# Performance work log

Hardware: AMD Instinct MI355X
Metric: run time of the kernel (lower is better)

The kernel has to match this reference:

```python
import math
import jax, jax.numpy as jnp
import numpy as np

D_MODEL = 512
N_HEADS = 8
NUM_PHASES = 3
LN_EPS = 1e-5


def setup_inputs() -> dict:
    key = jax.random.key(0)
    ks = jax.random.split(key, 8)
    B, T, C = 4, 2048, D_MODEL
    s = 1.0 / math.sqrt(C)  # keep activations sane
    return {
        "x": jax.random.normal(ks[0], (B, T, C), dtype=jnp.float32),
        "Wq_w": jax.random.normal(ks[1], (C, C), dtype=jnp.float32) * s,
        "Wq_b": jnp.zeros((C,), dtype=jnp.float32),
        "Wk_w": jax.random.normal(ks[2], (C, C), dtype=jnp.float32) * s,
        "Wk_b": jnp.zeros((C,), dtype=jnp.float32),
        "Wv_w": jax.random.normal(ks[3], (C, C), dtype=jnp.float32) * s,
        "Wv_b": jnp.zeros((C,), dtype=jnp.float32),
        "Wo_w": jax.random.normal(ks[4], (C, C), dtype=jnp.float32) * s,
        "Wo_b": jnp.zeros((C,), dtype=jnp.float32),
        "phase_bias": jax.random.normal(ks[5], (NUM_PHASES, NUM_PHASES), dtype=jnp.float32),
        "ln_g": jnp.ones((C,), dtype=jnp.float32),
        "ln_b": jnp.zeros((C,), dtype=jnp.float32),
    }


def reference(x, Wq_w, Wq_b, Wk_w, Wk_b, Wv_w, Wv_b, Wo_w, Wo_b, phase_bias, ln_g, ln_b):
    B, T, C = x.shape
    H, dk = N_HEADS, C // N_HEADS
    # torch Linear: y = x @ W.T + b
    Q = (x @ Wq_w.T + Wq_b).reshape(B, T, H, dk).transpose(0, 2, 1, 3)
    K = (x @ Wk_w.T + Wk_b).reshape(B, T, H, dk).transpose(0, 2, 1, 3)
    V = (x @ Wv_w.T + Wv_b).reshape(B, T, H, dk).transpose(0, 2, 1, 3)
    scores = jnp.einsum('bhqd,bhkd->bhqk', Q, K) / math.sqrt(dk)  # [B,H,T,T]
    # tiled additive phase bias (num_phases <= T)
    n_tiles = (T + NUM_PHASES - 1) // NUM_PHASES
    bias = jnp.tile(phase_bias, (n_tiles, n_tiles))[:T, :T]  # [T,T]
    scores = scores + bias  # broadcast over B,H
    attn = jax.nn.softmax(scores, axis=-1)  # dropout is identity in eval
    ctx = jnp.einsum('bhqk,bhkd->bhqd', attn, V)
    ctx = ctx.transpose(0, 2, 1, 3).reshape(B, T, C)
    out = ctx @ Wo_w.T + Wo_b
    y = out + x
    mu = jnp.mean(y, axis=-1, keepdims=True)
    var = jnp.mean(jnp.square(y - mu), axis=-1, keepdims=True)
    return (y - mu) / jnp.sqrt(var + LN_EPS) * ln_g + ln_b
```

## Files before the change

### kernel.cpp

```cpp
#include <hip/hip_runtime.h>

typedef __attribute__((ext_vector_type(8))) short s16x8;
typedef __attribute__((ext_vector_type(8))) unsigned short u16x8;
typedef __attribute__((ext_vector_type(4))) float f32x4;
typedef unsigned short u16;
typedef unsigned int u32;

#define T_ 2048
#define C_ 512
#define H_ 8
#define DKP 96
#define LOG2E 1.44269504088896340736f
#define QSCALE 0.18033688011112042f

__device__ __forceinline__ u16 f2b(float f) {
  u32 u = __float_as_uint(f);
  return (u16)((u + 0x7FFFu + ((u >> 16) & 1u)) >> 16);
}

__device__ __forceinline__ float b2f(u16 b) {
  return __uint_as_float(((u32)b) << 16);
}

__device__ __forceinline__ u16x8 cvt8(float4 a, float4 b) {
  u16x8 o;
  o[0] = f2b(a.x); o[1] = f2b(a.y); o[2] = f2b(a.z); o[3] = f2b(a.w);
  o[4] = f2b(b.x); o[5] = f2b(b.y); o[6] = f2b(b.z); o[7] = f2b(b.w);
  return o;
}

__device__ __forceinline__ f32x4 mfma16(s16x8 a, s16x8 b, f32x4 c) {
  return __builtin_amdgcn_mfma_f32_16x16x32_bf16(a, b, c, 0, 0, 0);
}

__global__ __launch_bounds__(256) void k_convert(
    const float* __restrict__ x,
    const float* __restrict__ wq, const float* __restrict__ wk,
    const float* __restrict__ wv, const float* __restrict__ wo,
    const float* __restrict__ bq, const float* __restrict__ bk,
    const float* __restrict__ bv, const float* __restrict__ pb,
    u16* __restrict__ xb, u16* __restrict__ wcat, u16* __restrict__ wo16,
    float* __restrict__ bcat, u16* __restrict__ qp, u16* __restrict__ kp)
{
  const int blk = blockIdx.x, tid = threadIdx.x;
  if (blk < 2048) {
    int i = blk * 2048 + tid * 8;
    float4 a = *(const float4*)(x + i);
    float4 b = *(const float4*)(x + i + 4);
    *(u16x8*)(xb + i) = cvt8(a, b);
  } else if (blk < 2432) {
    int bi = blk - 2048;
    const float* src; int off;
    if (bi < 128)      { src = wq; off = bi * 2048; }
    else if (bi < 256) { src = wk; off = (bi - 128) * 2048; }
    else               { src = wv; off = (bi - 256) * 2048; }
    int i = off + tid * 8;
    float4 a = *(const float4*)(src + i);
    float4 b = *(const float4*)(src + i + 4);
    *(u16x8*)(wcat + bi * 2048 + tid * 8) = cvt8(a, b);
  } else if (blk < 2560) {
    int i = (blk - 2432) * 2048 + tid * 8;
    float4 a = *(const float4*)(wo + i);
    float4 b = *(const float4*)(wo + i + 4);
    *(u16x8*)(wo16 + i) = cvt8(a, b);
  } else if (blk == 2560) {
    if (tid < 192) {
      int i = tid * 8;
      const float* src; int off;
      if (i < 512)       { src = bq; off = i; }
      else if (i < 1024) { src = bk; off = i - 512; }
      else               { src = bv; off = i - 1024; }
      *(float4*)(bcat + i)     = *(const float4*)(src + off);
      *(float4*)(bcat + i + 4) = *(const float4*)(src + off + 4);
    }
  } else if (blk < 3585) {
    int e = (blk - 2561) * 2048 + tid * 8;
    int row = e >> 5, cc = e & 31;
    int tp = (row & 2047) % 3;
    u16x8 o;
    #pragma unroll
    for (int j = 0; j < 8; ++j) {
      int cidx = cc + j;
      o[j] = (cidx < 3) ? ((tp == cidx) ? (u16)0x3F80 : (u16)0) : (u16)0;
    }
    *(u16x8*)(qp + row * DKP + 64 + cc) = o;
  } else {
    int e = (blk - 3585) * 2048 + tid * 8;
    int row = e >> 5, cc = e & 31;
    int tp = (row & 2047) % 3;
    u16x8 o;
    #pragma unroll
    for (int j = 0; j < 8; ++j) {
      int cidx = cc + j;
      o[j] = (cidx < 3) ? f2b(pb[cidx * 3 + tp] * LOG2E) : (u16)0;
    }
    *(u16x8*)(kp + row * DKP + 64 + cc) = o;
  }
}

template<int MODE>
__global__ __launch_bounds__(256) void k_gemm(
    const u16* __restrict__ A, const u16* __restrict__ Bw,
    const float* __restrict__ bias,
    u16* __restrict__ qp, u16* __restrict__ kp, u16* __restrict__ vtmp,
    float* __restrict__ yout)
{
  const int n0 = blockIdx.x * 128;
  const int m0 = blockIdx.y * 128;
  const int tid = threadIdx.x;
  const int lane = tid & 63, wid = tid >> 6;
  const int g = lane >> 4, c = lane & 15;
  const int wm = wid >> 1, wn = wid & 1;

  __shared__ alignas(16) u16 As[128 * 40];
  __shared__ alignas(16) u16 Bs[128 * 40];

  f32x4 acc[4][4];
  #pragma unroll
  for (int i = 0; i < 4; ++i)
    #pragma unroll
    for (int j = 0; j < 4; ++j) acc[i][j] = f32x4{0.f, 0.f, 0.f, 0.f};

  const int srow = tid >> 1;
  const int sj = (tid & 1) * 16;
  const u16* Ag = A + (m0 + srow) * C_ + sj;
  const u16* Bg = Bw + (n0 + srow) * C_ + sj;
  u16* Al = As + srow * 40 + sj;
  u16* Bl = Bs + srow * 40 + sj;

  s16x8 a0 = *(const s16x8*)(Ag);
  s16x8 a1 = *(const s16x8*)(Ag + 8);
  s16x8 b0 = *(const s16x8*)(Bg);
  s16x8 b1 = *(const s16x8*)(Bg + 8);

  const int KT = C_ / 32;
  for (int kt = 0; kt < KT; ++kt) {
    __syncthreads();
    *(s16x8*)(Al) = a0; *(s16x8*)(Al + 8) = a1;
    *(s16x8*)(Bl) = b0; *(s16x8*)(Bl + 8) = b1;
    __syncthreads();
    if (kt + 1 < KT) {
      a0 = *(const s16x8*)(Ag + (kt + 1) * 32);
      a1 = *(const s16x8*)(Ag + (kt + 1) * 32 + 8);
      b0 = *(const s16x8*)(Bg + (kt + 1) * 32);
      b1 = *(const s16x8*)(Bg + (kt + 1) * 32 + 8);
    }
    s16x8 af[4], bf[4];
    #pragma unroll
    for (int mf = 0; mf < 4; ++mf)
      af[mf] = *(const s16x8*)(As + (wm * 64 + mf * 16 + c) * 40 + g * 8);
    #pragma unroll
    for (int nf = 0; nf < 4; ++nf)
      bf[nf] = *(const s16x8*)(Bs + (wn * 64 + nf * 16 + c) * 40 + g * 8);
    #pragma unroll
    for (int mf = 0; mf < 4; ++mf)
      #pragma unroll
      for (int nf = 0; nf < 4; ++nf)
        acc[mf][nf] = mfma16(af[mf], bf[nf], acc[mf][nf]);
  }

  float bv4[4];
  #pragma unroll
  for (int nf = 0; nf < 4; ++nf) bv4[nf] = bias[n0 + wn * 64 + nf * 16 + c];

  #pragma unroll
  for (int mf = 0; mf < 4; ++mf) {
    const int btb = m0 + wm * 64 + mf * 16 + g * 4;
    #pragma unroll
    for (int nf = 0; nf < 4; ++nf) {
      const int n = n0 + wn * 64 + nf * 16 + c;
      #pragma unroll
      for (int r = 0; r < 4; ++r) {
        float v = acc[mf][nf][r] + bv4[nf];
        const int row = btb + r;
        if (MODE == 1) {
          yout[row * C_ + n] = v;
        } else {
          if (n < 512) {
            const int hh = n >> 6, d = n & 63;
            const int bb = row >> 11, t = row & 2047;
            qp[((bb * H_ + hh) * T_ + t) * DKP + d] = f2b(v * QSCALE);
          } else if (n < 1024) {
            const int nn = n - 512;
            const int hh = nn >> 6, d = nn & 63;
            const int bb = row >> 11, t = row & 2047;
            kp[((bb * H_ + hh) * T_ + t) * DKP + d] = f2b(v);
          } else {
            vtmp[row * C_ + (n - 1024)] = f2b(v);
          }
        }
      }
    }
  }
}

__global__ __launch_bounds__(256) void k_vtrans(const u16* __restrict__ vtmp,
                                                u16* __restrict__ vt)
{
  const int t0 = blockIdx.x * 64;
  const int bh = blockIdx.y;
  const int b = bh >> 3, h = bh & 7;
  const int tid = threadIdx.x;
  __shared__ alignas(16) u16 tile[64 * 72];
  #pragma unroll
  for (int it = 0; it < 2; ++it) {
    int task = tid + it * 256;
    int r = task >> 3, cj = task & 7;
    int pr = (r & 32) | (((r & 15) << 1) | ((r >> 4) & 1));
    u16x8 v = *(const u16x8*)(vtmp + (b * T_ + t0 + r) * C_ + h * 64 + cj * 8);
    #pragma unroll
    for (int j = 0; j < 8; ++j) tile[(cj * 8 + j) * 72 + pr] = v[j];
  }
  __syncthreads();
  #pragma unroll
  for (int it = 0; it < 2; ++it) {
    int task = tid + it * 256;
    int d = task >> 3, cj = task & 7;
    u16x8 o = *(const u16x8*)(tile + d * 72 + cj * 8);
    *(u16x8*)(vt + (bh * 80 + d) * T_ + t0 + cj * 8) = o;
  }
  if (tid < 128) {
    int d = 64 + (tid >> 3), cj = tid & 7;
    u16 val = (d == 64) ? (u16)0x3F80 : (u16)0;
    u16x8 o;
    #pragma unroll
    for (int j = 0; j < 8; ++j) o[j] = val;
    *(u16x8*)(vt + (bh * 80 + d) * T_ + t0 + cj * 8) = o;
  }
}

__global__ __launch_bounds__(256) void k_attn(
    const u16* __restrict__ qp, const u16* __restrict__ kp,
    const u16* __restrict__ vt, u16* __restrict__ pc0, u16* __restrict__ pc1,
    float* __restrict__ pl)
{
  const int lid = blockIdx.x;
  const int xcd = lid & 7, j = lid >> 3;
  const int gsel = j >> 4, qblk = j & 15;
  const int bhz = xcd * 8 + gsel;
  const int bh = bhz >> 1, z = bhz & 1;

  const int tid = threadIdx.x, wid = tid >> 6, lane = tid & 63;
  const int g = lane >> 4, c = lane & 15;

  __shared__ alignas(16) u16 Ks[32 * 104];
  __shared__ alignas(16) u16 Vs[80 * 40];
  __shared__ alignas(16) u16 Ps[4][32 * 40];

  const int q0 = qblk * 128 + wid * 32;
  const u16* qpb = qp + (bh * T_ + q0) * DKP;
  s16x8 qfr[2][3];
  #pragma unroll
  for (int a = 0; a < 2; ++a)
    #pragma unroll
    for (int ks = 0; ks < 3; ++ks)
      qfr[a][ks] = *(const s16x8*)(qpb + (a * 16 + c) * DKP + ks * 32 + g * 8);

  f32x4 acc[2][5];
  #pragma unroll
  for (int a = 0; a < 2; ++a)
    #pragma unroll
    for (int df = 0; df < 5; ++df) acc[a][df] = f32x4{0.f, 0.f, 0.f, 0.f};

  const int r_k0 = tid / 12, j_k0 = tid % 12;
  const int r_k1 = (256 + tid) / 12, j_k1 = (256 + tid) % 12;
  const bool k2 = tid < 128;
  const u16* kpb = kp + (bh * T_ + z * 1024) * DKP;
  u16* kl0 = Ks + r_k0 * 104 + j_k0 * 8;
  u16* kl1 = Ks + r_k1 * 104 + j_k1 * 8;
  const int ko0 = r_k0 * DKP + j_k0 * 8;
  const int ko1 = r_k1 * DKP + j_k1 * 8;

  const int r_v0 = tid >> 2, j_v0 = tid & 3;
  const bool v2 = tid < 64;
  const int r_v1 = 64 + (tid >> 2), j_v1 = tid & 3;
  const u16* vtb = vt + bh * 80 * T_ + z * 1024;
  u16* vl0 = Vs + r_v0 * 40 + j_v0 * 8;
  u16* vl1 = Vs + r_v1 * 40 + j_v1 * 8;
  const int vo0 = r_v0 * T_ + j_v0 * 8;
  const int vo1 = r_v1 * T_ + j_v1 * 8;

  s16x8 kc0 = *(const s16x8*)(kpb + ko0);
  s16x8 kc1 = {}; if (k2) kc1 = *(const s16x8*)(kpb + ko1);
  s16x8 vc0 = *(const s16x8*)(vtb + vo0);
  s16x8 vc1 = {}; if (v2) vc1 = *(const s16x8*)(vtb + vo1);

  for (int kt = 0; kt < 32; ++kt) {
    __syncthreads();
    *(s16x8*)kl0 = kc0;
    if (k2) *(s16x8*)kl1 = kc1;
    *(s16x8*)vl0 = vc0;
    if (v2) *(s16x8*)vl1 = vc1;
    __syncthreads();
    if (kt < 31) {
      const int off = (kt + 1) * 32;
      kc0 = *(const s16x8*)(kpb + off * DKP + ko0);
      if (k2) kc1 = *(const s16x8*)(kpb + off * DKP + ko1);
      vc0 = *(const s16x8*)(vtb + off + vo0);
      if (v2) vc1 = *(const s16x8*)(vtb + off + vo1);
    }

    f32x4 s2[2][2];
    #pragma unroll
    for (int a = 0; a < 2; ++a)
      #pragma unroll
      for (int kf = 0; kf < 2; ++kf) s2[a][kf] = f32x4{0.f, 0.f, 0.f, 0.f};
    #pragma unroll
    for (int kf = 0; kf < 2; ++kf)
      #pragma unroll
      for (int ks = 0; ks < 3; ++ks) {
        s16x8 kfrag = *(const s16x8*)(Ks + (kf * 16 + c) * 104 + (ks * 4 + g) * 8);
        s2[0][kf] = mfma16(qfr[0][ks], kfrag, s2[0][kf]);
        s2[1][kf] = mfma16(qfr[1][ks], kfrag, s2[1][kf]);
      }

    #pragma unroll
    for (int a = 0; a < 2; ++a) {
      u32* pw = (u32*)(Ps[wid] + (a * 16 + g * 4) * 40) + c;
      #pragma unroll
      for (int r = 0; r < 4; ++r) {
        u32 b0 = __float_as_uint(exp2f(s2[a][0][r]));
        u32 b1 = __float_as_uint(exp2f(s2[a][1][r]));
        pw[r * 20] = ((b0 + 0x8000u) >> 16) | (((b1 + 0x8000u) >> 16) << 16);
      }
    }

    s16x8 pf0 = *(const s16x8*)(Ps[wid] + c * 40 + g * 8);
    s16x8 pf1 = *(const s16x8*)(Ps[wid] + (16 + c) * 40 + g * 8);
    #pragma unroll
    for (int df = 0; df < 5; ++df) {
      s16x8 vfrag = *(const s16x8*)(Vs + (df * 16 + c) * 40 + g * 8);
      acc[0][df] = mfma16(pf0, vfrag, acc[0][df]);
      acc[1][df] = mfma16(pf1, vfrag, acc[1][df]);
    }
  }

  u16* pcz = z ? pc1 : pc0;
  float* plz = pl + z * 65536;
  #pragma unroll
  for (int a = 0; a < 2; ++a) {
    #pragma unroll
    for (int r = 0; r < 4; ++r) {
      const int trow = q0 + a * 16 + g * 4 + r;
      u16* outp = pcz + ((size_t)bh * T_ + trow) * 64;
      #pragma unroll
      for (int df = 0; df < 4; ++df)
        outp[df * 16 + c] = f2b(acc[a][df][r]);
      if (c == 0) plz[bh * T_ + trow] = acc[a][4][r];
    }
  }
}

__global__ __launch_bounds__(256) void k_combine(
    const u16* __restrict__ pc0, const u16* __restrict__ pc1,
    const float* __restrict__ pl, u16* __restrict__ ctxb)
{
  const int gid = blockIdx.x * 256 + threadIdx.x;
  const int row = gid >> 3;
  const int dj = (gid & 7) * 8;
  const u16x8 c0 = *(const u16x8*)(pc0 + (size_t)row * 64 + dj);
  const u16x8 c1 = *(const u16x8*)(pc1 + (size_t)row * 64 + dj);
  const float inv = 1.0f / (pl[row] + pl[65536 + row]);
  u16x8 o;
  #pragma unroll
  for (int j = 0; j < 8; ++j)
    o[j] = f2b((b2f(c0[j]) + b2f(c1[j])) * inv);
  const int bh = row >> 11, t = row & 2047;
  const int b = bh >> 3, h = bh & 7;
  *(u16x8*)(ctxb + ((size_t)(b * T_ + t)) * C_ + h * 64 + dj) = o;
}

__global__ __launch_bounds__(256) void k_ln(
    const float* __restrict__ yo, const float* __restrict__ x,
    const float* __restrict__ gg, const float* __restrict__ bb,
    float* __restrict__ out)
{
  const int row = blockIdx.x * 4 + (threadIdx.x >> 6);
  const int lane = threadIdx.x & 63;
  const float4* yp = (const float4*)(yo + row * C_);
  const float4* xp = (const float4*)(x + row * C_);
  float4 v[2];
  float s = 0.f, ss = 0.f;
  #pragma unroll
  for (int i = 0; i < 2; ++i) {
    float4 a = yp[lane * 2 + i];
    float4 xx = xp[lane * 2 + i];
    float4 w;
    w.x = a.x + xx.x; w.y = a.y + xx.y; w.z = a.z + xx.z; w.w = a.w + xx.w;
    v[i] = w;
    s += w.x + w.y + w.z + w.w;
    ss += w.x * w.x + w.y * w.y + w.z * w.z + w.w * w.w;
  }
  #pragma unroll
  for (int m = 1; m < 64; m <<= 1) {
    s += __shfl_xor(s, m);
    ss += __shfl_xor(ss, m);
  }
  const float mu = s * (1.0f / 512.0f);
  const float rs = rsqrtf(ss * (1.0f / 512.0f) - mu * mu + 1e-5f);
  const float4* gp = (const float4*)gg;
  const float4* bp = (const float4*)bb;
  float4* op = (float4*)(out + row * C_);
  #pragma unroll
  for (int i = 0; i < 2; ++i) {
    float4 gv = gp[lane * 2 + i], bv = bp[lane * 2 + i];
    float4 w = v[i], o;
    o.x = (w.x - mu) * rs * gv.x + bv.x;
    o.y = (w.y - mu) * rs * gv.y + bv.y;
    o.z = (w.z - mu) * rs * gv.z + bv.z;
    o.w = (w.w - mu) * rs * gv.w + bv.w;
    op[lane * 2 + i] = o;
  }
}

extern "C" void kernel_launch(void* const* d_in, const int* in_sizes, int n_in,
                              void* d_out, int out_size, void* d_ws, size_t ws_size,
                              hipStream_t stream)
{
  const float* x   = (const float*)d_in[0];
  const float* wqw = (const float*)d_in[1];
  const float* wqb = (const float*)d_in[2];
  const float* wkw = (const float*)d_in[3];
  const float* wkb = (const float*)d_in[4];
  const float* wvw = (const float*)d_in[5];
  const float* wvb = (const float*)d_in[6];
  const float* wow = (const float*)d_in[7];
  const float* wob = (const float*)d_in[8];
  const float* pb  = (const float*)d_in[9];
  const float* lng = (const float*)d_in[10];
  const float* lnb = (const float*)d_in[11];

  char* w = (char*)d_ws;
  u16*   xb   = (u16*)(w + 0);
  u16*   wcat = (u16*)(w + 8388608);
  u16*   wo16 = (u16*)(w + 9961472);
  float* bcat = (float*)(w + 10485760);
  u16*   qp   = (u16*)(w + 10491904);
  u16*   kp   = (u16*)(w + 23074816);
  u16*   vtmp = (u16*)(w + 35657728);
  u16*   vtq  = (u16*)(w + 44046336);
  u16*   ctxb = (u16*)(w + 54532096);
  float* yout = (float*)(w + 10491904);
  u16*   pc0  = xb;
  u16*   pc1  = vtmp;
  float* pl   = (float*)wcat;

  k_convert<<<4609, 256, 0, stream>>>(x, wqw, wkw, wvw, wow, wqb, wkb, wvb, pb,
                                      xb, wcat, wo16, bcat, qp, kp);
  k_gemm<0><<<dim3(12, 64), 256, 0, stream>>>(xb, wcat, bcat, qp, kp, vtmp, nullptr);
  k_vtrans<<<dim3(32, 32), 256, 0, stream>>>(vtmp, vtq);
  k_attn<<<1024, 256, 0, stream>>>(qp, kp, vtq, pc0, pc1, pl);
  k_combine<<<2048, 256, 0, stream>>>(pc0, pc1, pl, ctxb);
  k_gemm<1><<<dim3(4, 64), 256, 0, stream>>>(ctxb, wo16, wob, nullptr, nullptr, nullptr, yout);
  k_ln<<<2048, 256, 0, stream>>>(yout, x, lng, lnb, (float*)d_out);
}
```

Baseline: 235.6 us.

## Use direct global-to-LDS loads in GEMM and read K/V straight from global in attention

The GEMM now stages tiles with global_load_lds (direct global-to-shared copies) into an unpadded 32-wide layout. This replaces the register-prefetch double buffer, so there is no software prefetch overlap and the unpadded layout may cause LDS bank conflicts. The attention kernel drops its shared K/V staging and reads MFMA fragments directly from global memory, counting on cache hits across the four waves instead of LDS traffic and barriers. The softmax exp and bf16 packing now use the hardware exp2 builtin and a packed bf16 conversion instruction.

```diff
diff --git a/kernel.cpp b/kernel.cpp
--- a/kernel.cpp
+++ b/kernel.cpp
@@ -22,6 +22,12 @@
   return __uint_as_float(((u32)b) << 16);
 }
 
+__device__ __forceinline__ u32 cvtpk(float a, float b) {
+  u32 d;
+  asm("v_cvt_pk_bf16_f32 %0, %1, %2" : "=v"(d) : "v"(a), "v"(b));
+  return d;
+}
+
 __device__ __forceinline__ u16x8 cvt8(float4 a, float4 b) {
   u16x8 o;
   o[0] = f2b(a.x); o[1] = f2b(a.y); o[2] = f2b(a.z); o[3] = f2b(a.w);
@@ -32,6 +38,10 @@
 __device__ __forceinline__ f32x4 mfma16(s16x8 a, s16x8 b, f32x4 c) {
   return __builtin_amdgcn_mfma_f32_16x16x32_bf16(a, b, c, 0, 0, 0);
 }
+
+#define GLL(gp, lp) __builtin_amdgcn_global_load_lds( \
+    (const __attribute__((address_space(1))) unsigned int*)(gp), \
+    (__attribute__((address_space(3))) unsigned int*)(lp), 16, 0, 0)
 
 __global__ __launch_bounds__(256) void k_convert(
     const float* __restrict__ x,
@@ -112,8 +122,8 @@
   const int g = lane >> 4, c = lane & 15;
   const int wm = wid >> 1, wn = wid & 1;
 
-  __shared__ alignas(16) u16 As[128 * 40];
-  __shared__ alignas(16) u16 Bs[128 * 40];
+  __shared__ alignas(16) u16 As[128 * 32];
+  __shared__ alignas(16) u16 Bs[128 * 32];
 
   f32x4 acc[4][4];
   #pragma unroll
@@ -121,42 +131,35 @@
     #pragma unroll
     for (int j = 0; j < 4; ++j) acc[i][j] = f32x4{0.f, 0.f, 0.f, 0.f};
 
-  const int srow = tid >> 1;
-  const int sj = (tid & 1) * 16;
-  const u16* Ag = A + (m0 + srow) * C_ + sj;
-  const u16* Bg = Bw + (n0 + srow) * C_ + sj;
-  u16* Al = As + srow * 40 + sj;
-  u16* Bl = Bs + srow * 40 + sj;
-
-  s16x8 a0 = *(const s16x8*)(Ag);
-  s16x8 a1 = *(const s16x8*)(Ag + 8);
-  s16x8 b0 = *(const s16x8*)(Bg);
-  s16x8 b1 = *(const s16x8*)(Bg + 8);
+  const u16* Ag0 = A + (m0 + (tid >> 2)) * C_ + (tid & 3) * 8;
+  const u16* Ag1 = Ag0 + 64 * C_;
+  const u16* Bg0 = Bw + (n0 + (tid >> 2)) * C_ + (tid & 3) * 8;
+  const u16* Bg1 = Bg0 + 64 * C_;
+  u16* Al0 = As + tid * 8;
+  u16* Al1 = As + (256 + tid) * 8;
+  u16* Bl0 = Bs + tid * 8;
+  u16* Bl1 = Bs + (256 + tid) * 8;
 
   const int KT = C_ / 32;
   for (int kt = 0; kt < KT; ++kt) {
+    GLL(Ag0 + kt * 32, Al0);
+    GLL(Ag1 + kt * 32, Al1);
+    GLL(Bg0 + kt * 32, Bl0);
+    GLL(Bg1 + kt * 32, Bl1);
     __syncthreads();
-    *(s16x8*)(Al) = a0; *(s16x8*)(Al + 8) = a1;
-    *(s16x8*)(Bl) = b0; *(s16x8*)(Bl + 8) = b1;
-    __syncthreads();
-    if (kt + 1 < KT) {
-      a0 = *(const s16x8*)(Ag + (kt + 1) * 32);
-      a1 = *(const s16x8*)(Ag + (kt + 1) * 32 + 8);
-      b0 = *(const s16x8*)(Bg + (kt + 1) * 32);
-      b1 = *(const s16x8*)(Bg + (kt + 1) * 32 + 8);
-    }
     s16x8 af[4], bf[4];
     #pragma unroll
     for (int mf = 0; mf < 4; ++mf)
-      af[mf] = *(const s16x8*)(As + (wm * 64 + mf * 16 + c) * 40 + g * 8);
+      af[mf] = *(const s16x8*)(As + (wm * 64 + mf * 16 + c) * 32 + g * 8);
     #pragma unroll
     for (int nf = 0; nf < 4; ++nf)
-      bf[nf] = *(const s16x8*)(Bs + (wn * 64 + nf * 16 + c) * 40 + g * 8);
+      bf[nf] = *(const s16x8*)(Bs + (wn * 64 + nf * 16 + c) * 32 + g * 8);
     #pragma unroll
     for (int mf = 0; mf < 4; ++mf)
       #pragma unroll
       for (int nf = 0; nf < 4; ++nf)
         acc[mf][nf] = mfma16(af[mf], bf[nf], acc[mf][nf]);
+    __syncthreads();
   }
 
   float bv4[4];
@@ -243,8 +246,6 @@
   const int tid = threadIdx.x, wid = tid >> 6, lane = tid & 63;
   const int g = lane >> 4, c = lane & 15;
 
-  __shared__ alignas(16) u16 Ks[32 * 104];
-  __shared__ alignas(16) u16 Vs[80 * 40];
   __shared__ alignas(16) u16 Ps[4][32 * 40];
 
   const int q0 = qblk * 128 + wid * 32;
@@ -262,43 +263,12 @@
     #pragma unroll
     for (int df = 0; df < 5; ++df) acc[a][df] = f32x4{0.f, 0.f, 0.f, 0.f};
 
-  const int r_k0 = tid / 12, j_k0 = tid % 12;
-  const int r_k1 = (256 + tid) / 12, j_k1 = (256 + tid) % 12;
-  const bool k2 = tid < 128;
-  const u16* kpb = kp + (bh * T_ + z * 1024) * DKP;
-  u16* kl0 = Ks + r_k0 * 104 + j_k0 * 8;
-  u16* kl1 = Ks + r_k1 * 104 + j_k1 * 8;
-  const int ko0 = r_k0 * DKP + j_k0 * 8;
-  const int ko1 = r_k1 * DKP + j_k1 * 8;
-
-  const int r_v0 = tid >> 2, j_v0 = tid & 3;
-  const bool v2 = tid < 64;
-  const int r_v1 = 64 + (tid >> 2), j_v1 = tid & 3;
-  const u16* vtb = vt + bh * 80 * T_ + z * 1024;
-  u16* vl0 = Vs + r_v0 * 40 + j_v0 * 8;
-  u16* vl1 = Vs + r_v1 * 40 + j_v1 * 8;
-  const int vo0 = r_v0 * T_ + j_v0 * 8;
-  const int vo1 = r_v1 * T_ + j_v1 * 8;
-
-  s16x8 kc0 = *(const s16x8*)(kpb + ko0);
-  s16x8 kc1 = {}; if (k2) kc1 = *(const s16x8*)(kpb + ko1);
-  s16x8 vc0 = *(const s16x8*)(vtb + vo0);
-  s16x8 vc1 = {}; if (v2) vc1 = *(const s16x8*)(vtb + vo1);
+  const u16* kpt = kp + ((size_t)bh * T_ + z * 1024) * DKP;
+  const u16* vpt = vt + (size_t)bh * 80 * T_ + z * 1024;
 
   for (int kt = 0; kt < 32; ++kt) {
-    __syncthreads();
-    *(s16x8*)kl0 = kc0;
-    if (k2) *(s16x8*)kl1 = kc1;
-    *(s16x8*)vl0 = vc0;
-    if (v2) *(s16x8*)vl1 = vc1;
-    __syncthreads();
-    if (kt < 31) {
-      const int off = (kt + 1) * 32;
-      kc0 = *(const s16x8*)(kpb + off * DKP + ko0);
-      if (k2) kc1 = *(const s16x8*)(kpb + off * DKP + ko1);
-      vc0 = *(const s16x8*)(vtb + off + vo0);
-      if (v2) vc1 = *(const s16x8*)(vtb + off + vo1);
-    }
+    const u16* kb = kpt + kt * (32 * DKP);
+    const u16* vb = vpt + kt * 32;
 
     f32x4 s2[2][2];
     #pragma unroll
@@ -309,7 +279,7 @@
     for (int kf = 0; kf < 2; ++kf)
       #pragma unroll
       for (int ks = 0; ks < 3; ++ks) {
-        s16x8 kfrag = *(const s16x8*)(Ks + (kf * 16 + c) * 104 + (ks * 4 + g) * 8);
+        s16x8 kfrag = *(const s16x8*)(kb + (kf * 16 + c) * DKP + ks * 32 + g * 8);
         s2[0][kf] = mfma16(qfr[0][ks], kfrag, s2[0][kf]);
         s2[1][kf] = mfma16(qfr[1][ks], kfrag, s2[1][kf]);
       }
@@ -319,9 +289,9 @@
       u32* pw = (u32*)(Ps[wid] + (a * 16 + g * 4) * 40) + c;
       #pragma unroll
       for (int r = 0; r < 4; ++r) {
-        u32 b0 = __float_as_uint(exp2f(s2[a][0][r]));
-        u32 b1 = __float_as_uint(exp2f(s2[a][1][r]));
-        pw[r * 20] = ((b0 + 0x8000u) >> 16) | (((b1 + 0x8000u) >> 16) << 16);
+        float e0 = __builtin_amdgcn_exp2f(s2[a][0][r]);
+        float e1 = __builtin_amdgcn_exp2f(s2[a][1][r]);
+        pw[r * 20] = cvtpk(e0, e1);
       }
     }
 
@@ -329,7 +299,7 @@
     s16x8 pf1 = *(const s16x8*)(Ps[wid] + (16 + c) * 40 + g * 8);
     #pragma unroll
     for (int df = 0; df < 5; ++df) {
-      s16x8 vfrag = *(const s16x8*)(Vs + (df * 16 + c) * 40 + g * 8);
+      s16x8 vfrag = *(const s16x8*)(vb + (df * 16 + c) * T_ + g * 8);
       acc[0][df] = mfma16(pf0, vfrag, acc[0][df]);
       acc[1][df] = mfma16(pf1, vfrag, acc[1][df]);
     }
```

After: 267.3 us. +13.5%, slower.
